# Kernel optimization log

Hardware: AMD Instinct MI355X
Metric: run time of the kernel (lower is better)

The kernel has to match this reference:

```python
import jax, jax.numpy as jnp
import numpy as np

N = 10000
E = 160000
IN_CH = 128
EMB = 64
HEADS = 12
NEG_SLOPE = 0.2


def setup_inputs() -> dict:
    key = jax.random.key(0)
    ks = jax.random.split(key, 8)
    x = jax.random.normal(ks[0], (N, IN_CH), dtype=jnp.float32)
    edge_index = jax.random.randint(ks[1], (2, E), 0, N, dtype=jnp.int32)
    # embedding Linear params
    We = jax.random.normal(ks[2], (IN_CH, EMB), dtype=jnp.float32) / np.sqrt(IN_CH)
    be = jnp.zeros((EMB,), dtype=jnp.float32)
    # GATConv params (heads=12, out_channels=EMB per head, concat=False -> mean)
    W = jax.random.normal(ks[3], (EMB, HEADS * EMB), dtype=jnp.float32) / np.sqrt(EMB)
    att_src = jax.random.normal(ks[4], (HEADS, EMB), dtype=jnp.float32) / np.sqrt(EMB)
    att_dst = jax.random.normal(ks[5], (HEADS, EMB), dtype=jnp.float32) / np.sqrt(EMB)
    bias = jnp.zeros((EMB,), dtype=jnp.float32)
    return {"x": x, "edge_index": edge_index, "We": We, "be": be,
            "W": W, "att_src": att_src, "att_dst": att_dst, "bias": bias}


def _gat_conv(h, edge_index, W, att_src, att_dst, bias):
    n = h.shape[0]
    # project to per-head features: [N, H, D]
    hh = (h @ W).reshape(n, HEADS, EMB)
    a_src = jnp.einsum('nhd,hd->nh', hh, att_src)  # [N, H]
    a_dst = jnp.einsum('nhd,hd->nh', hh, att_dst)  # [N, H]
    # add self loops (PyG default add_self_loops=True)
    loops = jnp.arange(n, dtype=edge_index.dtype)
    src = jnp.concatenate([edge_index[0], loops])
    dst = jnp.concatenate([edge_index[1], loops])
    # per-edge attention logits, leaky relu
    e = a_src[src] + a_dst[dst]                     # [E', H]
    e = jnp.where(e > 0, e, NEG_SLOPE * e)
    # segment softmax over incoming edges of each dst node
    emax = jax.ops.segment_max(e, dst, num_segments=n)
    e = jnp.exp(e - emax[dst])
    denom = jax.ops.segment_sum(e, dst, num_segments=n)
    alpha = e / (denom[dst] + 1e-16)                # [E', H]
    # weighted scatter-add of source features
    msg = hh[src] * alpha[:, :, None]               # [E', H, D]
    out = jax.ops.segment_sum(msg, dst, num_segments=n)  # [N, H, D]
    return out.mean(axis=1) + bias                  # concat=False -> mean heads


def reference(x, edge_index, We, be, W, att_src, att_dst, bias):
    emb = jax.nn.relu(x @ We + be)                  # [N, EMB]
    y = _gat_conv(emb, edge_index, W, att_src, att_dst, bias)
    return jax.nn.relu(emb + y)
```

## Files before the change

kernel.cpp:

```cpp
#include <hip/hip_runtime.h>
#include <hip/hip_fp16.h>
#include <math.h>

#define N_NODES 10000
#define N_EDGES 160000
#define IN_CH 128
#define EMB 64
#define HEADS 12
#define NEG_SLOPE 0.2f
#define DEGMAX 64
#define POISON_I ((int)0xAAAAAAAA)

typedef float v2f __attribute__((ext_vector_type(2)));
typedef short bf16x8 __attribute__((ext_vector_type(8)));
typedef float f32x4 __attribute__((ext_vector_type(4)));

__device__ __forceinline__ unsigned short f2bf(float f) {
  unsigned u = __float_as_uint(f);
  return (unsigned short)((u + 0x7FFFu + ((u >> 16) & 1u)) >> 16);
}

__global__ __launch_bounds__(768) void fused_embed_project(
    const float* __restrict__ x, const int* __restrict__ ei,
    const float* __restrict__ We, const float* __restrict__ be,
    const float* __restrict__ W, const float* __restrict__ att_src,
    const float* __restrict__ att_dst,
    float* __restrict__ emb, unsigned char* __restrict__ hh8,
    float* __restrict__ a_src, float* __restrict__ a_dst,
    int* __restrict__ deg, int* __restrict__ csr) {
  const int tid = threadIdx.x;
  const int lane = tid & 63;
  const int c = tid >> 6;
  const int mt = __builtin_amdgcn_readfirstlane(blockIdx.x);
  const int q = lane & 15, sg = lane >> 4;

  if (tid < 256) {
    const int e = mt * 256 + tid;
    const int src = ei[e];
    const int dst = ei[N_EDGES + e];
    const int pos = atomicAdd(&deg[dst], 1) - POISON_I;
    if ((unsigned)pos < (unsigned)DEGMAX) csr[(dst << 6) + pos] = src;
  }

  __shared__ unsigned short xs[16 * 128];
  __shared__ unsigned short embb_s[16 * 64];

  if (tid < 512) {
    const int i = tid >> 5;
    const int d = (tid & 31) << 2;
    const float4 xv = *(const float4*)&x[(long)(mt * 16 + i) * IN_CH + d];
    unsigned short* dp = xs + i * 128 + (((d >> 3) ^ (i & 7)) << 3) + (d & 7);
    dp[0] = f2bf(xv.x); dp[1] = f2bf(xv.y);
    dp[2] = f2bf(xv.z); dp[3] = f2bf(xv.w);
  }

  bf16x8 b0[4], b1[4];
  if (c >= 4) {
    #pragma unroll
    for (int nt = 0; nt < 4; ++nt) {
      const float* wp0 = W + (sg * 8) * (HEADS * EMB) + c * 64 + nt * 16 + q;
      #pragma unroll
      for (int j = 0; j < 8; ++j) {
        b0[nt][j] = (short)f2bf(wp0[j * (HEADS * EMB)]);
        b1[nt][j] = (short)f2bf(wp0[(32 + j) * (HEADS * EMB)]);
      }
    }
  }

  bf16x8 bw[4];
  if (c < 4) {
    #pragma unroll
    for (int ks = 0; ks < 4; ++ks) {
      const float* wep = We + (ks * 32 + sg * 8) * EMB + c * 16 + q;
      #pragma unroll
      for (int j = 0; j < 8; ++j) bw[ks][j] = (short)f2bf(wep[j * EMB]);
    }
  }

  __syncthreads();

  if (c < 4) {
    f32x4 z = {0.f, 0.f, 0.f, 0.f};
    #pragma unroll
    for (int ks = 0; ks < 4; ++ks) {
      const bf16x8 a =
          *(const bf16x8*)(xs + q * 128 + ((((ks * 4 + sg) << 3)) ^ ((q & 7) << 3)));
      z = __builtin_amdgcn_mfma_f32_16x16x32_bf16(a, bw[ks], z, 0, 0, 0);
    }
    const float bq = be[c * 16 + q];
    const int dim = c * 16 + q;
    #pragma unroll
    for (int r = 0; r < 4; ++r) {
      const int node = sg * 4 + r;
      const float v = fmaxf(z[r] + bq, 0.f);
      emb[(mt * 16 + node) * EMB + dim] = v;
      embb_s[node * 64 + (dim ^ ((node & 7) << 3))] = f2bf(v);
    }
    #pragma unroll
    for (int nt = 0; nt < 4; ++nt) {
      const float* wp0 = W + (sg * 8) * (HEADS * EMB) + c * 64 + nt * 16 + q;
      #pragma unroll
      for (int j = 0; j < 8; ++j) {
        b0[nt][j] = (short)f2bf(wp0[j * (HEADS * EMB)]);
        b1[nt][j] = (short)f2bf(wp0[(32 + j) * (HEADS * EMB)]);
      }
    }
  }

  __syncthreads();

  const bf16x8 a0 = *(const bf16x8*)(embb_s + q * 64 + ((sg * 8) ^ ((q & 7) << 3)));
  const bf16x8 a1 = *(const bf16x8*)(embb_s + q * 64 + (((4 + sg) * 8) ^ ((q & 7) << 3)));

  f32x4 acc[4];
  #pragma unroll
  for (int nt = 0; nt < 4; ++nt) {
    f32x4 z = {0.f, 0.f, 0.f, 0.f};
    z = __builtin_amdgcn_mfma_f32_16x16x32_bf16(a0, b0[nt], z, 0, 0, 0);
    z = __builtin_amdgcn_mfma_f32_16x16x32_bf16(a1, b1[nt], z, 0, 0, 0);
    acc[nt] = z;
  }

  float as[4], ad[4];
  #pragma unroll
  for (int nt = 0; nt < 4; ++nt) {
    as[nt] = att_src[c * 64 + q + 16 * nt];
    ad[nt] = att_dst[c * 64 + q + 16 * nt];
  }

  float ps[4], pd[4];
  #pragma unroll
  for (int r = 0; r < 4; ++r) {
    const int node = mt * 16 + sg * 4 + r;
    int pk = __builtin_amdgcn_cvt_pk_fp8_f32(acc[0][r], acc[1][r], 0, false);
    pk = __builtin_amdgcn_cvt_pk_fp8_f32(acc[2][r], acc[3][r], pk, true);
    *(int*)(hh8 + (long)node * (HEADS * EMB) + c * 64 + (q << 2)) = pk;
    ps[r] = acc[0][r] * as[0] + acc[1][r] * as[1] + acc[2][r] * as[2] + acc[3][r] * as[3];
    pd[r] = acc[0][r] * ad[0] + acc[1][r] * ad[1] + acc[2][r] * ad[2] + acc[3][r] * ad[3];
  }
  #pragma unroll
  for (int off = 1; off < 16; off <<= 1) {
    #pragma unroll
    for (int r = 0; r < 4; ++r) {
      ps[r] += __shfl_xor(ps[r], off, 64);
      pd[r] += __shfl_xor(pd[r], off, 64);
    }
  }
  if (q == 0) {
    #pragma unroll
    for (int r = 0; r < 4; ++r) {
      const int node = mt * 16 + sg * 4 + r;
      a_src[node * HEADS + c] = ps[r];
      a_dst[node * HEADS + c] = pd[r];
    }
  }
}

__global__ __launch_bounds__(256) void gat_gather(
    const unsigned char* __restrict__ hh8, const float* __restrict__ a_src,
    const float* __restrict__ a_dst, const float* __restrict__ emb,
    const float* __restrict__ bias, const int* __restrict__ deg_arr,
    const int* __restrict__ csr, float* __restrict__ out) {
  const int lane = threadIdx.x & 63;
  const int wv = threadIdx.x >> 6;
  const int n = blockIdx.x * 4 + wv;
  const int sub = lane >> 4;
  const int q = lane & 15;

  __shared__ int   srcs_s[4][64];
  __shared__ float w_s[4][768];
  __shared__ float inv_s[4][HEADS];

  const int rdeg = min(deg_arr[n] - POISON_I, DEGMAX - 1);
  const int csz = rdeg + 1;

  srcs_s[wv][lane] = (lane < rdeg) ? csr[(n << 6) + lane] : n;

  const int P = csz * 12;
  for (int p = lane; p < P; p += 64) {
    const int e = (p * 683) >> 13;
    const int h = p - e * 12;
    float lg = a_src[srcs_s[wv][e] * HEADS + h] + a_dst[n * HEADS + h];
    lg = (lg > 0.f) ? lg : NEG_SLOPE * lg;
    w_s[wv][p] = __expf(lg);
  }

  if (lane < HEADS) {
    float dn = 0.f;
    for (int e = 0; e < csz; ++e) dn += w_s[wv][e * 12 + lane];
    inv_s[wv][lane] = 1.f / (dn + 1e-16f);
  }

  float4 a0 = make_float4(0.f, 0.f, 0.f, 0.f);
  float4 a1 = make_float4(0.f, 0.f, 0.f, 0.f);
  float4 a2 = make_float4(0.f, 0.f, 0.f, 0.f);
  const int boff = lane << 2;
  #pragma unroll 4
  for (int e = 0; e < csz; ++e) {
    const unsigned char* row = hh8 + (long)srcs_s[wv][e] * (HEADS * EMB);
    const unsigned d0 = *(const unsigned*)(row + boff);
    const unsigned d1 = *(const unsigned*)(row + 256 + boff);
    const unsigned d2 = *(const unsigned*)(row + 512 + boff);
    const int wb = e * 12 + sub;
    const float w0 = w_s[wv][wb];
    const float w1 = w_s[wv][wb + 4];
    const float w2 = w_s[wv][wb + 8];
    v2f lo, hi;
    lo = __builtin_amdgcn_cvt_pk_f32_fp8(d0, false);
    hi = __builtin_amdgcn_cvt_pk_f32_fp8(d0, true);
    a0.x = fmaf(w0, lo.x, a0.x); a0.y = fmaf(w0, lo.y, a0.y);
    a0.z = fmaf(w0, hi.x, a0.z); a0.w = fmaf(w0, hi.y, a0.w);
    lo = __builtin_amdgcn_cvt_pk_f32_fp8(d1, false);
    hi = __builtin_amdgcn_cvt_pk_f32_fp8(d1, true);
    a1.x = fmaf(w1, lo.x, a1.x); a1.y = fmaf(w1, lo.y, a1.y);
    a1.z = fmaf(w1, hi.x, a1.z); a1.w = fmaf(w1, hi.y, a1.w);
    lo = __builtin_amdgcn_cvt_pk_f32_fp8(d2, false);
    hi = __builtin_amdgcn_cvt_pk_f32_fp8(d2, true);
    a2.x = fmaf(w2, lo.x, a2.x); a2.y = fmaf(w2, lo.y, a2.y);
    a2.z = fmaf(w2, hi.x, a2.z); a2.w = fmaf(w2, hi.y, a2.w);
  }

  const float i0 = inv_s[wv][sub];
  const float i1 = inv_s[wv][4 + sub];
  const float i2 = inv_s[wv][8 + sub];
  w_s[wv][sub * 64 + q]      = a0.x * i0;
  w_s[wv][sub * 64 + q + 16] = a0.y * i0;
  w_s[wv][sub * 64 + q + 32] = a0.z * i0;
  w_s[wv][sub * 64 + q + 48] = a0.w * i0;
  w_s[wv][(4 + sub) * 64 + q]      = a1.x * i1;
  w_s[wv][(4 + sub) * 64 + q + 16] = a1.y * i1;
  w_s[wv][(4 + sub) * 64 + q + 32] = a1.z * i1;
  w_s[wv][(4 + sub) * 64 + q + 48] = a1.w * i1;
  w_s[wv][(8 + sub) * 64 + q]      = a2.x * i2;
  w_s[wv][(8 + sub) * 64 + q + 16] = a2.y * i2;
  w_s[wv][(8 + sub) * 64 + q + 32] = a2.z * i2;
  w_s[wv][(8 + sub) * 64 + q + 48] = a2.w * i2;

  float s = 0.f;
  #pragma unroll
  for (int h = 0; h < HEADS; ++h) s += w_s[wv][h * 64 + lane];
  const float yv = s * (1.f / HEADS) + bias[lane];
  out[n * EMB + lane] = fmaxf(emb[n * EMB + lane] + yv, 0.f);
}

extern "C" void kernel_launch(void* const* d_in, const int* in_sizes, int n_in,
                              void* d_out, int out_size, void* d_ws, size_t ws_size,
                              hipStream_t stream) {
  const float* x       = (const float*)d_in[0];
  const int*   ei      = (const int*)  d_in[1];
  const float* We      = (const float*)d_in[2];
  const float* be      = (const float*)d_in[3];
  const float* W       = (const float*)d_in[4];
  const float* att_src = (const float*)d_in[5];
  const float* att_dst = (const float*)d_in[6];
  const float* bias    = (const float*)d_in[7];
  float* out = (float*)d_out;

  float* emb    = (float*)d_ws;
  float* a_src  = emb + (long)N_NODES * EMB;
  float* a_dst  = a_src + N_NODES * HEADS;
  int*   deg    = (int*)(a_dst + N_NODES * HEADS);
  int*   csr    = deg + N_NODES;
  unsigned char* hh8 = (unsigned char*)(csr + N_NODES * DEGMAX);

  fused_embed_project<<<625, 768, 0, stream>>>(
      x, ei, We, be, W, att_src, att_dst, emb, hh8, a_src, a_dst, deg, csr);
  gat_gather<<<N_NODES / 4, 256, 0, stream>>>(hh8, a_src, a_dst, emb, bias, deg, csr, out);
}
```

Baseline: 114.7 us.

## Aggregate bf16 embeddings per head before projecting, then project with MFMA

Instead of projecting every node to 12 heads and gathering the large fp8 projected rows per edge, the gather kernel now aggregates the small bf16 embedding rows with per-head attention weights. A new kernel then applies the per-head weight matrix to the aggregated features via MFMA, averages heads, and applies the residual and ReLU. This cuts per-edge gather bytes substantially. In exchange it writes and rereads a per-node 12x64 bf16 intermediate and adds a third launch.

```diff
diff --git a/kernel.cpp b/kernel.cpp
--- a/kernel.cpp
+++ b/kernel.cpp
@@ -11,13 +11,16 @@
 #define DEGMAX 64
 #define POISON_I ((int)0xAAAAAAAA)
 
-typedef float v2f __attribute__((ext_vector_type(2)));
 typedef short bf16x8 __attribute__((ext_vector_type(8)));
 typedef float f32x4 __attribute__((ext_vector_type(4)));
 
 __device__ __forceinline__ unsigned short f2bf(float f) {
   unsigned u = __float_as_uint(f);
   return (unsigned short)((u + 0x7FFFu + ((u >> 16) & 1u)) >> 16);
+}
+
+__device__ __forceinline__ float bf2f(unsigned short us) {
+  return __uint_as_float((unsigned)us << 16);
 }
 
 __global__ __launch_bounds__(768) void fused_embed_project(
@@ -25,7 +28,7 @@
     const float* __restrict__ We, const float* __restrict__ be,
     const float* __restrict__ W, const float* __restrict__ att_src,
     const float* __restrict__ att_dst,
-    float* __restrict__ emb, unsigned char* __restrict__ hh8,
+    float* __restrict__ emb, unsigned short* __restrict__ embb,
     float* __restrict__ a_src, float* __restrict__ a_dst,
     int* __restrict__ deg, int* __restrict__ csr) {
   const int tid = threadIdx.x;
@@ -94,7 +97,9 @@
       const int node = sg * 4 + r;
       const float v = fmaxf(z[r] + bq, 0.f);
       emb[(mt * 16 + node) * EMB + dim] = v;
-      embb_s[node * 64 + (dim ^ ((node & 7) << 3))] = f2bf(v);
+      const unsigned short vb = f2bf(v);
+      embb[(mt * 16 + node) * EMB + dim] = vb;
+      embb_s[node * 64 + (dim ^ ((node & 7) << 3))] = vb;
     }
     #pragma unroll
     for (int nt = 0; nt < 4; ++nt) {
@@ -131,10 +136,6 @@
   float ps[4], pd[4];
   #pragma unroll
   for (int r = 0; r < 4; ++r) {
-    const int node = mt * 16 + sg * 4 + r;
-    int pk = __builtin_amdgcn_cvt_pk_fp8_f32(acc[0][r], acc[1][r], 0, false);
-    pk = __builtin_amdgcn_cvt_pk_fp8_f32(acc[2][r], acc[3][r], pk, true);
-    *(int*)(hh8 + (long)node * (HEADS * EMB) + c * 64 + (q << 2)) = pk;
     ps[r] = acc[0][r] * as[0] + acc[1][r] * as[1] + acc[2][r] * as[2] + acc[3][r] * as[3];
     pd[r] = acc[0][r] * ad[0] + acc[1][r] * ad[1] + acc[2][r] * ad[2] + acc[3][r] * ad[3];
   }
@@ -156,16 +157,13 @@
   }
 }
 
-__global__ __launch_bounds__(256) void gat_gather(
-    const unsigned char* __restrict__ hh8, const float* __restrict__ a_src,
-    const float* __restrict__ a_dst, const float* __restrict__ emb,
-    const float* __restrict__ bias, const int* __restrict__ deg_arr,
-    const int* __restrict__ csr, float* __restrict__ out) {
+__global__ __launch_bounds__(256) void gat_aggregate(
+    const unsigned short* __restrict__ embb, const float* __restrict__ a_src,
+    const float* __restrict__ a_dst, const int* __restrict__ deg_arr,
+    const int* __restrict__ csr, unsigned short* __restrict__ sagg) {
   const int lane = threadIdx.x & 63;
   const int wv = threadIdx.x >> 6;
   const int n = blockIdx.x * 4 + wv;
-  const int sub = lane >> 4;
-  const int q = lane & 15;
 
   __shared__ int   srcs_s[4][64];
   __shared__ float w_s[4][768];
@@ -191,56 +189,70 @@
     inv_s[wv][lane] = 1.f / (dn + 1e-16f);
   }
 
-  float4 a0 = make_float4(0.f, 0.f, 0.f, 0.f);
-  float4 a1 = make_float4(0.f, 0.f, 0.f, 0.f);
-  float4 a2 = make_float4(0.f, 0.f, 0.f, 0.f);
-  const int boff = lane << 2;
+  float s[12];
+  #pragma unroll
+  for (int h = 0; h < 12; ++h) s[h] = 0.f;
   #pragma unroll 4
   for (int e = 0; e < csz; ++e) {
-    const unsigned char* row = hh8 + (long)srcs_s[wv][e] * (HEADS * EMB);
-    const unsigned d0 = *(const unsigned*)(row + boff);
-    const unsigned d1 = *(const unsigned*)(row + 256 + boff);
-    const unsigned d2 = *(const unsigned*)(row + 512 + boff);
-    const int wb = e * 12 + sub;
-    const float w0 = w_s[wv][wb];
-    const float w1 = w_s[wv][wb + 4];
-    const float w2 = w_s[wv][wb + 8];
-    v2f lo, hi;
-    lo = __builtin_amdgcn_cvt_pk_f32_fp8(d0, false);
-    hi = __builtin_amdgcn_cvt_pk_f32_fp8(d0, true);
-    a0.x = fmaf(w0, lo.x, a0.x); a0.y = fmaf(w0, lo.y, a0.y);
-    a0.z = fmaf(w0, hi.x, a0.z); a0.w = fmaf(w0, hi.y, a0.w);
-    lo = __builtin_amdgcn_cvt_pk_f32_fp8(d1, false);
-    hi = __builtin_amdgcn_cvt_pk_f32_fp8(d1, true);
-    a1.x = fmaf(w1, lo.x, a1.x); a1.y = fmaf(w1, lo.y, a1.y);
-    a1.z = fmaf(w1, hi.x, a1.z); a1.w = fmaf(w1, hi.y, a1.w);
-    lo = __builtin_amdgcn_cvt_pk_f32_fp8(d2, false);
-    hi = __builtin_amdgcn_cvt_pk_f32_fp8(d2, true);
-    a2.x = fmaf(w2, lo.x, a2.x); a2.y = fmaf(w2, lo.y, a2.y);
-    a2.z = fmaf(w2, hi.x, a2.z); a2.w = fmaf(w2, hi.y, a2.w);
-  }
-
-  const float i0 = inv_s[wv][sub];
-  const float i1 = inv_s[wv][4 + sub];
-  const float i2 = inv_s[wv][8 + sub];
-  w_s[wv][sub * 64 + q]      = a0.x * i0;
-  w_s[wv][sub * 64 + q + 16] = a0.y * i0;
-  w_s[wv][sub * 64 + q + 32] = a0.z * i0;
-  w_s[wv][sub * 64 + q + 48] = a0.w * i0;
-  w_s[wv][(4 + sub) * 64 + q]      = a1.x * i1;
-  w_s[wv][(4 + sub) * 64 + q + 16] = a1.y * i1;
-  w_s[wv][(4 + sub) * 64 + q + 32] = a1.z * i1;
-  w_s[wv][(4 + sub) * 64 + q + 48] = a1.w * i1;
-  w_s[wv][(8 + sub) * 64 + q]      = a2.x * i2;
-  w_s[wv][(8 + sub) * 64 + q + 16] = a2.y * i2;
-  w_s[wv][(8 + sub) * 64 + q + 32] = a2.z * i2;
-  w_s[wv][(8 + sub) * 64 + q + 48] = a2.w * i2;
-
-  float s = 0.f;
-  #pragma unroll
-  for (int h = 0; h < HEADS; ++h) s += w_s[wv][h * 64 + lane];
-  const float yv = s * (1.f / HEADS) + bias[lane];
-  out[n * EMB + lane] = fmaxf(emb[n * EMB + lane] + yv, 0.f);
+    const float v = bf2f(embb[srcs_s[wv][e] * EMB + lane]);
+    const float* wp = w_s[wv] + e * 12;
+    #pragma unroll
+    for (int hp = 0; hp < 6; ++hp) {
+      const float2 w2 = *(const float2*)(wp + 2 * hp);
+      s[2 * hp]     = fmaf(w2.x, v, s[2 * hp]);
+      s[2 * hp + 1] = fmaf(w2.y, v, s[2 * hp + 1]);
+    }
+  }
+
+  #pragma unroll
+  for (int h = 0; h < 12; ++h)
+    sagg[(n * 12 + h) * 64 + lane] = f2bf(s[h] * inv_s[wv][h]);
+}
+
+__global__ __launch_bounds__(768) void project_out(
+    const unsigned short* __restrict__ sagg, const float* __restrict__ W,
+    const float* __restrict__ bias, const float* __restrict__ emb,
+    float* __restrict__ out) {
+  const int tid = threadIdx.x;
+  const int lane = tid & 63;
+  const int h = tid >> 6;
+  const int mt = __builtin_amdgcn_readfirstlane(blockIdx.x);
+  const int q = lane & 15, sg = lane >> 4;
+
+  __shared__ float proj[12][16][65];
+
+  const unsigned short* ar = sagg + ((mt * 16 + q) * 12 + h) * 64 + sg * 8;
+  const bf16x8 a0 = *(const bf16x8*)(ar);
+  const bf16x8 a1 = *(const bf16x8*)(ar + 32);
+
+  #pragma unroll
+  for (int nt = 0; nt < 4; ++nt) {
+    const float* wp0 = W + (sg * 8) * (HEADS * EMB) + h * 64 + nt * 16 + q;
+    bf16x8 b0, b1;
+    #pragma unroll
+    for (int j = 0; j < 8; ++j) {
+      b0[j] = (short)f2bf(wp0[j * (HEADS * EMB)]);
+      b1[j] = (short)f2bf(wp0[(32 + j) * (HEADS * EMB)]);
+    }
+    f32x4 z = {0.f, 0.f, 0.f, 0.f};
+    z = __builtin_amdgcn_mfma_f32_16x16x32_bf16(a0, b0, z, 0, 0, 0);
+    z = __builtin_amdgcn_mfma_f32_16x16x32_bf16(a1, b1, z, 0, 0, 0);
+    #pragma unroll
+    for (int r = 0; r < 4; ++r)
+      proj[h][sg * 4 + r][q + 16 * nt] = z[r];
+  }
+  __syncthreads();
+
+  for (int p = tid; p < 16 * EMB; p += 768) {
+    const int node = p >> 6;
+    const int dim = p & 63;
+    float sum = 0.f;
+    #pragma unroll
+    for (int hh = 0; hh < 12; ++hh) sum += proj[hh][node][dim];
+    const float yv = sum * (1.f / HEADS) + bias[dim];
+    const int n = mt * 16 + node;
+    out[n * EMB + dim] = fmaxf(emb[n * EMB + dim] + yv, 0.f);
+  }
 }
 
 extern "C" void kernel_launch(void* const* d_in, const int* in_sizes, int n_in,
@@ -261,9 +273,11 @@
   float* a_dst  = a_src + N_NODES * HEADS;
   int*   deg    = (int*)(a_dst + N_NODES * HEADS);
   int*   csr    = deg + N_NODES;
-  unsigned char* hh8 = (unsigned char*)(csr + N_NODES * DEGMAX);
+  unsigned short* embb = (unsigned short*)(csr + N_NODES * DEGMAX);
+  unsigned short* sagg = embb + (long)N_NODES * EMB;
 
   fused_embed_project<<<625, 768, 0, stream>>>(
-      x, ei, We, be, W, att_src, att_dst, emb, hh8, a_src, a_dst, deg, csr);
-  gat_gather<<<N_NODES / 4, 256, 0, stream>>>(hh8, a_src, a_dst, emb, bias, deg, csr, out);
-}
+      x, ei, We, be, W, att_src, att_dst, emb, embb, a_src, a_dst, deg, csr);
+  gat_aggregate<<<N_NODES / 4, 256, 0, stream>>>(embb, a_src, a_dst, deg, csr, sagg);
+  project_out<<<625, 768, 0, stream>>>(sagg, W, bias, emb, out);
+}
```

After: 121.4 us. 5.8% more time.
